# Optimization experiments

Measured on AMD Instinct MI355X. Metric: run time of the kernel, lower is better.

The kernel has to match this reference:

```python
import jax, jax.numpy as jnp
import numpy as np

B, L, D, H, UNITS = 64, 4096, 512, 512, 256

def setup_inputs() -> dict:
    key = jax.random.key(0)
    ks = jax.random.split(key, 8)
    s = lambda fan_in: 1.0 / np.sqrt(fan_in)
    return {
        "features": jax.random.normal(ks[0], (B, L, D), dtype=jnp.float32),
        "hidden": jax.random.normal(ks[1], (B, H), dtype=jnp.float32),
        "W1_k": jax.random.uniform(ks[2], (D, UNITS), jnp.float32, -s(D), s(D)),
        "W1_b": jnp.zeros((UNITS,), jnp.float32),
        "W2_k": jax.random.uniform(ks[3], (H, UNITS), jnp.float32, -s(H), s(H)),
        "W2_b": jnp.zeros((UNITS,), jnp.float32),
        "V_k": jax.random.uniform(ks[4], (UNITS, 1), jnp.float32, -s(UNITS), s(UNITS)),
        "V_b": jnp.zeros((1,), jnp.float32),
    }

def reference(features, hidden, W1_k, W1_b, W2_k, W2_b, V_k, V_b):
    # features: [B, L, D], hidden: [B, H]
    f_proj = jnp.einsum('bld,du->blu', features, W1_k) + W1_b          # [B, L, U]
    h_proj = (hidden @ W2_k + W2_b)[:, None, :]                        # [B, 1, U]
    score = jnp.einsum('blu,uo->blo', jnp.tanh(f_proj + h_proj), V_k) + V_b  # [B, L, 1]
    attention_weights = jax.nn.softmax(score, axis=1)                  # [B, L, 1]
    context_vector = jnp.sum(attention_weights * features, axis=1)     # [B, D]
    return (context_vector, attention_weights)
```

## Files before the change

kernel.cpp:

```cpp
#include <hip/hip_runtime.h>

#define Bsz 64
#define Lsz 4096
#define Dsz 512
#define Hsz 512
#define Usz 256
#define LT  64
#define NLB (Lsz / LT)

typedef __attribute__((ext_vector_type(8))) short s8v;
typedef __attribute__((ext_vector_type(4))) float f4v;
typedef __attribute__((ext_vector_type(8))) unsigned short u16x8;

#define SW(r, c) (((((c) >> 3) ^ ((r) & 7)) << 3) | ((c) & 7))

__device__ __forceinline__ unsigned short f2bf(float f) {
    unsigned int u = __float_as_uint(f);
    u += 0x7FFFu + ((u >> 16) & 1u);
    return (unsigned short)(u >> 16);
}
__device__ __forceinline__ float bf2f(unsigned int lo16) {
    return __uint_as_float(lo16 << 16);
}
__device__ __forceinline__ void barrier_lds() {
    asm volatile("s_waitcnt lgkmcnt(0)" ::: "memory");
    __builtin_amdgcn_s_barrier();
}


__global__ __launch_bounds__(256) void k_prep(const float* __restrict__ W1,
                                              const float* __restrict__ hidden,
                                              const float* __restrict__ W2,
                                              unsigned short* __restrict__ W1T,
                                              float* __restrict__ hp_part,
                                              float* __restrict__ den,
                                              float* __restrict__ ctx_acc) {
    int blk = blockIdx.x, tid = threadIdx.x;
    if (blk < 32) {
        __shared__ unsigned short Lt[64][72];
        int kb = blk >> 2, ub = blk & 3;
        {
            int rr = tid >> 2, c16 = (tid & 3) * 16;
            const float* src = W1 + (size_t)(kb * 64 + rr) * Usz + ub * 64 + c16;
            f4v v0 = *reinterpret_cast<const f4v*>(src);
            f4v v1 = *reinterpret_cast<const f4v*>(src + 4);
            f4v v2 = *reinterpret_cast<const f4v*>(src + 8);
            f4v v3 = *reinterpret_cast<const f4v*>(src + 12);
            u16x8 o0 = { f2bf(v0.x), f2bf(v0.y), f2bf(v0.z), f2bf(v0.w),
                         f2bf(v1.x), f2bf(v1.y), f2bf(v1.z), f2bf(v1.w) };
            u16x8 o1 = { f2bf(v2.x), f2bf(v2.y), f2bf(v2.z), f2bf(v2.w),
                         f2bf(v3.x), f2bf(v3.y), f2bf(v3.z), f2bf(v3.w) };
            *reinterpret_cast<u16x8*>(&Lt[rr][c16])     = o0;
            *reinterpret_cast<u16x8*>(&Lt[rr][c16 + 8]) = o1;
        }
        __syncthreads();
        {
            int ur = tid >> 2, k16 = (tid & 3) * 16;
            u16x8 o0, o1;
#pragma unroll
            for (int i = 0; i < 8; ++i) o0[i] = Lt[k16 + i][ur];
#pragma unroll
            for (int i = 0; i < 8; ++i) o1[i] = Lt[k16 + 8 + i][ur];
            unsigned short* dst = W1T + (size_t)(ub * 64 + ur) * Dsz + kb * 64 + k16;
            *reinterpret_cast<u16x8*>(dst)     = o0;
            *reinterpret_cast<u16x8*>(dst + 8) = o1;
        }
    } else if (blk < 288) {
        int idx = blk - 32;
        int kq = idx >> 6, b = idx & 63;
        const float* hrow = hidden + (size_t)b * Hsz + kq * 128;
        const float* w2p  = W2 + (size_t)(kq * 128) * Usz + tid;
        float a0 = 0.f, a1 = 0.f, a2 = 0.f, a3 = 0.f;
#pragma unroll 8
        for (int k = 0; k < 128; k += 4) {
            a0 = fmaf(hrow[k + 0], w2p[(size_t)(k + 0) * Usz], a0);
            a1 = fmaf(hrow[k + 1], w2p[(size_t)(k + 1) * Usz], a1);
            a2 = fmaf(hrow[k + 2], w2p[(size_t)(k + 2) * Usz], a2);
            a3 = fmaf(hrow[k + 3], w2p[(size_t)(k + 3) * Usz], a3);
        }
        hp_part[((size_t)kq * Bsz + b) * Usz + tid] = (a0 + a1) + (a2 + a3);
    } else {
        int b = blk - 288;
        if (tid == 0) den[b] = 0.f;
        ctx_acc[b * Dsz + tid] = 0.f;
        ctx_acc[b * Dsz + 256 + tid] = 0.f;
    }
}

__global__ void __launch_bounds__(512)
__attribute__((amdgpu_waves_per_eu(4, 4))) k_score_ctx(
    const float* __restrict__ feat, const unsigned short* __restrict__ W1T,
    const float* __restrict__ hp_part, const float* __restrict__ W1b,
    const float* __restrict__ W2b, const float* __restrict__ Vk,
    const float* __restrict__ Vb, float* __restrict__ el_arr,
    float* __restrict__ den, float* __restrict__ ctx_acc)
{
    __shared__ __align__(16) unsigned short A[LT][Dsz];
    __shared__ float hp[Usz], vv[Usz];
    __shared__ float spart[8][LT];
    __shared__ float el[LT];
    __shared__ float pc[2][Dsz];

    const int tid  = threadIdx.x;
    const int w    = tid >> 6;
    const int lane = tid & 63;
    const int lr   = lane & 15;
    const int lg   = lane >> 4;
    const int b    = blockIdx.x >> 6;
    const int lb   = blockIdx.x & 63;
    const int l0   = lb * LT;

    const int srow = tid >> 3;
    const int sfc  = (tid & 7) * 16;
    const float* fb = feat + ((size_t)b * Lsz + l0 + srow) * Dsz + sfc;

    f4v st[2][4];
#pragma unroll
    for (int i = 0; i < 4; ++i) st[0][i] = *reinterpret_cast<const f4v*>(fb + i * 4);
#pragma unroll
    for (int i = 0; i < 4; ++i) st[1][i] = *reinterpret_cast<const f4v*>(fb + 128 + i * 4);
    __builtin_amdgcn_sched_barrier(0);

    if (tid < Usz) {
        const float* hpb = hp_part + (size_t)b * Usz + tid;
        hp[tid] = (hpb[0] + hpb[Bsz * Usz]) + (hpb[2 * Bsz * Usz] + hpb[3 * Bsz * Usz])
                + W1b[tid] + W2b[tid];
        vv[tid] = Vk[tid];
    }
    {
        u16x8 o0 = { f2bf(st[0][0].x), f2bf(st[0][0].y), f2bf(st[0][0].z), f2bf(st[0][0].w),
                     f2bf(st[0][1].x), f2bf(st[0][1].y), f2bf(st[0][1].z), f2bf(st[0][1].w) };
        u16x8 o1 = { f2bf(st[0][2].x), f2bf(st[0][2].y), f2bf(st[0][2].z), f2bf(st[0][2].w),
                     f2bf(st[0][3].x), f2bf(st[0][3].y), f2bf(st[0][3].z), f2bf(st[0][3].w) };
        *reinterpret_cast<u16x8*>(&A[srow][SW(srow, sfc)])     = o0;
        *reinterpret_cast<u16x8*>(&A[srow][SW(srow, sfc + 8)]) = o1;
    }
    barrier_lds();

    const unsigned short* bp0 = W1T + (size_t)(w * 32 + lr) * Dsz + lg * 8;
    const unsigned short* bp1 = bp0 + 16 * Dsz;
    f4v acc[4][2];
#pragma unroll
    for (int mf = 0; mf < 4; ++mf) {
        acc[mf][0] = (f4v){0.f, 0.f, 0.f, 0.f};
        acc[mf][1] = (f4v){0.f, 0.f, 0.f, 0.f};
    }

#pragma unroll
    for (int c = 0; c < 4; ++c) {
        s8v bq[4][2];
#pragma unroll
        for (int k = 0; k < 4; ++k) {
            bq[k][0] = *reinterpret_cast<const s8v*>(bp0 + (c * 4 + k) * 32);
            bq[k][1] = *reinterpret_cast<const s8v*>(bp1 + (c * 4 + k) * 32);
        }
        __builtin_amdgcn_sched_barrier(0);
        if (c < 2) {
#pragma unroll
            for (int i = 0; i < 4; ++i)
                st[c & 1][i] = *reinterpret_cast<const f4v*>(fb + (c + 2) * 128 + i * 4);
        }
        __builtin_amdgcn_sched_barrier(0);
#pragma unroll
        for (int k = 0; k < 4; ++k) {
            const int kof = (c * 4 + k) * 32 + lg * 8;
#pragma unroll
            for (int mf = 0; mf < 4; ++mf) {
                const int row = mf * 16 + lr;
                s8v a = *reinterpret_cast<const s8v*>(&A[row][SW(row, kof)]);
                acc[mf][0] = __builtin_amdgcn_mfma_f32_16x16x32_bf16(a, bq[k][0], acc[mf][0], 0, 0, 0);
                acc[mf][1] = __builtin_amdgcn_mfma_f32_16x16x32_bf16(a, bq[k][1], acc[mf][1], 0, 0, 0);
            }
        }
        __builtin_amdgcn_sched_barrier(0);
        if (c < 3) {
            const int cc = (c + 1) * 128 + sfc;
            const f4v* s = st[(c + 1) & 1];
            u16x8 o0 = { f2bf(s[0].x), f2bf(s[0].y), f2bf(s[0].z), f2bf(s[0].w),
                         f2bf(s[1].x), f2bf(s[1].y), f2bf(s[1].z), f2bf(s[1].w) };
            u16x8 o1 = { f2bf(s[2].x), f2bf(s[2].y), f2bf(s[2].z), f2bf(s[2].w),
                         f2bf(s[3].x), f2bf(s[3].y), f2bf(s[3].z), f2bf(s[3].w) };
            *reinterpret_cast<u16x8*>(&A[srow][SW(srow, cc)])     = o0;
            *reinterpret_cast<u16x8*>(&A[srow][SW(srow, cc + 8)]) = o1;
            barrier_lds();
        }
    }

    {
        float rs[4][4];
#pragma unroll
        for (int mf = 0; mf < 4; ++mf)
#pragma unroll
            for (int r = 0; r < 4; ++r) rs[mf][r] = 0.f;
#pragma unroll
        for (int mf = 0; mf < 4; ++mf)
#pragma unroll
            for (int nf = 0; nf < 2; ++nf) {
                int col = w * 32 + nf * 16 + lr;
                float hpv = hp[col], vvv = vv[col];
#pragma unroll
                for (int r = 0; r < 4; ++r) {
                    float x = acc[mf][nf][r] + hpv;
                    float e = __expf(2.f * x);
                    rs[mf][r] = fmaf(1.f - 2.f / (e + 1.f), vvv, rs[mf][r]);
                }
            }
#pragma unroll
        for (int off = 1; off < 16; off <<= 1)
#pragma unroll
            for (int mf = 0; mf < 4; ++mf)
#pragma unroll
                for (int r = 0; r < 4; ++r)
                    rs[mf][r] += __shfl_xor(rs[mf][r], off, 64);
        if (lr == 0)
#pragma unroll
            for (int mf = 0; mf < 4; ++mf)
#pragma unroll
                for (int r = 0; r < 4; ++r)
                    spart[w][mf * 16 + lg * 4 + r] = rs[mf][r];
    }
    barrier_lds();

    if (tid < LT) {
        float s = Vb[0];
#pragma unroll
        for (int ww = 0; ww < 8; ++ww) s += spart[ww][tid];
        float e = __expf(s);
        el[tid] = e;
        el_arr[(size_t)b * Lsz + l0 + tid] = e;
        float es = e;
#pragma unroll
        for (int off = 1; off < 64; off <<= 1) es += __shfl_xor(es, off, 64);
        if (tid == 0) atomicAdd(&den[b], es);
    }
    barrier_lds();

    {
        const int qr = tid >> 8;
        const int d0 = (tid & 255) * 2;
        float a0 = 0.f, a1 = 0.f;
#pragma unroll 8
        for (int li = 0; li < 32; ++li) {
            int l = qr * 32 + li;
            unsigned int pk = *reinterpret_cast<const unsigned int*>(&A[l][SW(l, d0)]);
            float e = el[l];
            a0 = fmaf(e, bf2f(pk & 0xFFFFu), a0);
            a1 = fmaf(e, bf2f(pk >> 16), a1);
        }
        pc[qr][d0]     = a0;
        pc[qr][d0 + 1] = a1;
    }
    barrier_lds();
    atomicAdd(&ctx_acc[b * Dsz + tid], pc[0][tid] + pc[1][tid]);
}

__global__ __launch_bounds__(256) void k_finalize(const float* __restrict__ el_arr,
                                                  const float* __restrict__ den,
                                                  const float* __restrict__ ctx_acc,
                                                  float* __restrict__ ctx,
                                                  float* __restrict__ wout) {
    int blk = blockIdx.x, tid = threadIdx.x;
    int b = blk >> 2, q = blk & 3;
    float inv = 1.f / den[b];
    size_t base = (size_t)b * Lsz + q * 1024 + tid * 4;
    f4v e4 = *reinterpret_cast<const f4v*>(&el_arr[base]);
    f4v w4 = { e4.x * inv, e4.y * inv, e4.z * inv, e4.w * inv };
    *reinterpret_cast<f4v*>(&wout[base]) = w4;
    if (tid < 128) {
        int d = q * 128 + tid;
        ctx[(size_t)b * Dsz + d] = ctx_acc[b * Dsz + d] * inv;
    }
}

extern "C" void kernel_launch(void* const* d_in, const int* in_sizes, int n_in,
                              void* d_out, int out_size, void* d_ws, size_t ws_size,
                              hipStream_t stream) {
    const float* feat   = (const float*)d_in[0];
    const float* hidden = (const float*)d_in[1];
    const float* W1     = (const float*)d_in[2];
    const float* W1b    = (const float*)d_in[3];
    const float* W2     = (const float*)d_in[4];
    const float* W2b    = (const float*)d_in[5];
    const float* Vk     = (const float*)d_in[6];
    const float* Vb     = (const float*)d_in[7];

    unsigned short* w1t = (unsigned short*)d_ws;
    float* hp_part = (float*)((char*)d_ws + 256 * 1024);
    float* el_arr  = (float*)((char*)d_ws + 512 * 1024);
    float* den     = (float*)((char*)d_ws + 1536 * 1024);
    float* ctx_acc = (float*)((char*)d_ws + 1536 * 1024 + 256);

    float* ctx  = (float*)d_out;
    float* wout = ctx + Bsz * Dsz;

    k_prep<<<352, 256, 0, stream>>>(W1, hidden, W2, w1t, hp_part, den, ctx_acc);
    k_score_ctx<<<Bsz * NLB, 512, 0, stream>>>(feat, w1t, hp_part, W1b, W2b,
                                               Vk, Vb, el_arr, den, ctx_acc);
    k_finalize<<<Bsz * 4, 256, 0, stream>>>(el_arr, den, ctx_acc, ctx, wout);
}
```

Measured before the change: 194.6 us.

## Make score kernel persistent over 16 L-tiles with prefetched feature loads

Replaces the one-block-per-64-row grid (4096 blocks) with 512 blocks that each loop over 16 tiles of 32 rows. The next tile's features are prefetched into registers while the current tile's MFMAs run, and the W1 fragments are double-buffered. Context and denominator partials stay in registers across tiles, which cuts the number of atomics per batch. In exchange, the grid shrinks to 512 blocks, which may underfill the GPU's CUs, and each tile now pays several barriers and re-reads W1 from cache.

```diff
diff --git a/kernel.cpp b/kernel.cpp
--- a/kernel.cpp
+++ b/kernel.cpp
@@ -5,8 +5,9 @@
 #define Dsz 512
 #define Hsz 512
 #define Usz 256
-#define LT  64
-#define NLB (Lsz / LT)
+#define LT  32
+#define TPB 16
+#define NQB 8
 
 typedef __attribute__((ext_vector_type(8))) short s8v;
 typedef __attribute__((ext_vector_type(4))) float f4v;
@@ -87,6 +88,33 @@
     }
 }
 
+#define LOADB(dst, g)                                                          \
+    {                                                                          \
+        dst[0] = *reinterpret_cast<const s8v*>(bp0 + (2 * (g)) * 32);          \
+        dst[1] = *reinterpret_cast<const s8v*>(bp1 + (2 * (g)) * 32);          \
+        dst[2] = *reinterpret_cast<const s8v*>(bp0 + (2 * (g) + 1) * 32);      \
+        dst[3] = *reinterpret_cast<const s8v*>(bp1 + (2 * (g) + 1) * 32);      \
+    }
+
+#define GEMM2(ks, c0, c1)                                                      \
+    {                                                                          \
+        const int kof = (ks) * 32 + lg * 8;                                    \
+        s8v a0 = *reinterpret_cast<const s8v*>(&A[lr][SW(lr, kof)]);           \
+        s8v a1 = *reinterpret_cast<const s8v*>(&A[16 + lr][SW(16 + lr, kof)]); \
+        acc00 = __builtin_amdgcn_mfma_f32_16x16x32_bf16(a0, c0, acc00, 0, 0, 0); \
+        acc01 = __builtin_amdgcn_mfma_f32_16x16x32_bf16(a0, c1, acc01, 0, 0, 0); \
+        acc10 = __builtin_amdgcn_mfma_f32_16x16x32_bf16(a1, c0, acc10, 0, 0, 0); \
+        acc11 = __builtin_amdgcn_mfma_f32_16x16x32_bf16(a1, c1, acc11, 0, 0, 0); \
+    }
+
+#define GROUP(g, cur, nxt)                                                     \
+    {                                                                          \
+        if ((g) < 7) LOADB(nxt, (g) + 1);                                      \
+        __builtin_amdgcn_sched_barrier(0);                                     \
+        GEMM2(2 * (g),     cur[0], cur[1]);                                    \
+        GEMM2(2 * (g) + 1, cur[2], cur[3]);                                    \
+    }
+
 __global__ void __launch_bounds__(512)
 __attribute__((amdgpu_waves_per_eu(4, 4))) k_score_ctx(
     const float* __restrict__ feat, const unsigned short* __restrict__ W1T,
@@ -106,20 +134,8 @@
     const int lane = tid & 63;
     const int lr   = lane & 15;
     const int lg   = lane >> 4;
-    const int b    = blockIdx.x >> 6;
-    const int lb   = blockIdx.x & 63;
-    const int l0   = lb * LT;
-
-    const int srow = tid >> 3;
-    const int sfc  = (tid & 7) * 16;
-    const float* fb = feat + ((size_t)b * Lsz + l0 + srow) * Dsz + sfc;
-
-    f4v st[2][4];
-#pragma unroll
-    for (int i = 0; i < 4; ++i) st[0][i] = *reinterpret_cast<const f4v*>(fb + i * 4);
-#pragma unroll
-    for (int i = 0; i < 4; ++i) st[1][i] = *reinterpret_cast<const f4v*>(fb + 128 + i * 4);
-    __builtin_amdgcn_sched_barrier(0);
+    const int b    = blockIdx.x >> 3;
+    const int q8   = blockIdx.x & 7;
 
     if (tid < Usz) {
         const float* hpb = hp_part + (size_t)b * Usz + tid;
@@ -127,129 +143,134 @@
                 + W1b[tid] + W2b[tid];
         vv[tid] = Vk[tid];
     }
+
+    const int srow = tid >> 4;
+    const int sfc  = (tid & 15) * 32;
+    const float* fb = feat + ((size_t)b * Lsz + q8 * (TPB * LT) + srow) * Dsz + sfc;
+
+    f4v st[8];
+#pragma unroll
+    for (int i = 0; i < 8; ++i) st[i] = *reinterpret_cast<const f4v*>(fb + i * 4);
     {
-        u16x8 o0 = { f2bf(st[0][0].x), f2bf(st[0][0].y), f2bf(st[0][0].z), f2bf(st[0][0].w),
-                     f2bf(st[0][1].x), f2bf(st[0][1].y), f2bf(st[0][1].z), f2bf(st[0][1].w) };
-        u16x8 o1 = { f2bf(st[0][2].x), f2bf(st[0][2].y), f2bf(st[0][2].z), f2bf(st[0][2].w),
-                     f2bf(st[0][3].x), f2bf(st[0][3].y), f2bf(st[0][3].z), f2bf(st[0][3].w) };
-        *reinterpret_cast<u16x8*>(&A[srow][SW(srow, sfc)])     = o0;
-        *reinterpret_cast<u16x8*>(&A[srow][SW(srow, sfc + 8)]) = o1;
+#pragma unroll
+        for (int j = 0; j < 4; ++j) {
+            u16x8 o = { f2bf(st[2 * j].x),     f2bf(st[2 * j].y),
+                        f2bf(st[2 * j].z),     f2bf(st[2 * j].w),
+                        f2bf(st[2 * j + 1].x), f2bf(st[2 * j + 1].y),
+                        f2bf(st[2 * j + 1].z), f2bf(st[2 * j + 1].w) };
+            *reinterpret_cast<u16x8*>(&A[srow][SW(srow, sfc + j * 8)]) = o;
+        }
     }
     barrier_lds();
 
     const unsigned short* bp0 = W1T + (size_t)(w * 32 + lr) * Dsz + lg * 8;
     const unsigned short* bp1 = bp0 + 16 * Dsz;
-    f4v acc[4][2];
-#pragma unroll
-    for (int mf = 0; mf < 4; ++mf) {
-        acc[mf][0] = (f4v){0.f, 0.f, 0.f, 0.f};
-        acc[mf][1] = (f4v){0.f, 0.f, 0.f, 0.f};
-    }
-
-#pragma unroll
-    for (int c = 0; c < 4; ++c) {
-        s8v bq[4][2];
-#pragma unroll
-        for (int k = 0; k < 4; ++k) {
-            bq[k][0] = *reinterpret_cast<const s8v*>(bp0 + (c * 4 + k) * 32);
-            bq[k][1] = *reinterpret_cast<const s8v*>(bp1 + (c * 4 + k) * 32);
-        }
+
+    float cacc0 = 0.f, cacc1 = 0.f;
+    float dsum  = 0.f;
+    const int half = tid >> 8;
+    const int d0   = (tid & 255) * 2;
+
+#pragma unroll 1
+    for (int t = 0; t < TPB; ++t) {
+        f4v acc00 = (f4v){0.f, 0.f, 0.f, 0.f}, acc01 = (f4v){0.f, 0.f, 0.f, 0.f};
+        f4v acc10 = (f4v){0.f, 0.f, 0.f, 0.f}, acc11 = (f4v){0.f, 0.f, 0.f, 0.f};
+
+        s8v bq0[4], bq1[4];
+        LOADB(bq0, 0);
         __builtin_amdgcn_sched_barrier(0);
-        if (c < 2) {
-#pragma unroll
-            for (int i = 0; i < 4; ++i)
-                st[c & 1][i] = *reinterpret_cast<const f4v*>(fb + (c + 2) * 128 + i * 4);
+        if (t < TPB - 1) {
+#pragma unroll
+            for (int i = 0; i < 8; ++i)
+                st[i] = *reinterpret_cast<const f4v*>(fb + (size_t)(t + 1) * LT * Dsz + i * 4);
         }
         __builtin_amdgcn_sched_barrier(0);
-#pragma unroll
-        for (int k = 0; k < 4; ++k) {
-            const int kof = (c * 4 + k) * 32 + lg * 8;
-#pragma unroll
-            for (int mf = 0; mf < 4; ++mf) {
-                const int row = mf * 16 + lr;
-                s8v a = *reinterpret_cast<const s8v*>(&A[row][SW(row, kof)]);
-                acc[mf][0] = __builtin_amdgcn_mfma_f32_16x16x32_bf16(a, bq[k][0], acc[mf][0], 0, 0, 0);
-                acc[mf][1] = __builtin_amdgcn_mfma_f32_16x16x32_bf16(a, bq[k][1], acc[mf][1], 0, 0, 0);
-            }
-        }
-        __builtin_amdgcn_sched_barrier(0);
-        if (c < 3) {
-            const int cc = (c + 1) * 128 + sfc;
-            const f4v* s = st[(c + 1) & 1];
-            u16x8 o0 = { f2bf(s[0].x), f2bf(s[0].y), f2bf(s[0].z), f2bf(s[0].w),
-                         f2bf(s[1].x), f2bf(s[1].y), f2bf(s[1].z), f2bf(s[1].w) };
-            u16x8 o1 = { f2bf(s[2].x), f2bf(s[2].y), f2bf(s[2].z), f2bf(s[2].w),
-                         f2bf(s[3].x), f2bf(s[3].y), f2bf(s[3].z), f2bf(s[3].w) };
-            *reinterpret_cast<u16x8*>(&A[srow][SW(srow, cc)])     = o0;
-            *reinterpret_cast<u16x8*>(&A[srow][SW(srow, cc + 8)]) = o1;
-            barrier_lds();
-        }
-    }
-
-    {
-        float rs[4][4];
-#pragma unroll
-        for (int mf = 0; mf < 4; ++mf)
-#pragma unroll
-            for (int r = 0; r < 4; ++r) rs[mf][r] = 0.f;
-#pragma unroll
-        for (int mf = 0; mf < 4; ++mf)
-#pragma unroll
-            for (int nf = 0; nf < 2; ++nf) {
-                int col = w * 32 + nf * 16 + lr;
-                float hpv = hp[col], vvv = vv[col];
-#pragma unroll
-                for (int r = 0; r < 4; ++r) {
-                    float x = acc[mf][nf][r] + hpv;
+
+        GROUP(0, bq0, bq1); GROUP(1, bq1, bq0);
+        GROUP(2, bq0, bq1); GROUP(3, bq1, bq0);
+        GROUP(4, bq0, bq1); GROUP(5, bq1, bq0);
+        GROUP(6, bq0, bq1); GROUP(7, bq1, bq0);
+
+        {
+            float rs[2][4];
+#pragma unroll
+            for (int r = 0; r < 4; ++r) {
+                {
+                    int col = w * 32 + lr;
+                    float x = acc00[r] + hp[col];
                     float e = __expf(2.f * x);
-                    rs[mf][r] = fmaf(1.f - 2.f / (e + 1.f), vvv, rs[mf][r]);
+                    rs[0][r] = (1.f - 2.f / (e + 1.f)) * vv[col];
+                    x = acc01[r] + hp[col + 16];
+                    e = __expf(2.f * x);
+                    rs[0][r] = fmaf(1.f - 2.f / (e + 1.f), vv[col + 16], rs[0][r]);
+                }
+                {
+                    int col = w * 32 + lr;
+                    float x = acc10[r] + hp[col];
+                    float e = __expf(2.f * x);
+                    rs[1][r] = (1.f - 2.f / (e + 1.f)) * vv[col];
+                    x = acc11[r] + hp[col + 16];
+                    e = __expf(2.f * x);
+                    rs[1][r] = fmaf(1.f - 2.f / (e + 1.f), vv[col + 16], rs[1][r]);
                 }
             }
 #pragma unroll
-        for (int off = 1; off < 16; off <<= 1)
-#pragma unroll
-            for (int mf = 0; mf < 4; ++mf)
-#pragma unroll
-                for (int r = 0; r < 4; ++r)
-                    rs[mf][r] += __shfl_xor(rs[mf][r], off, 64);
-        if (lr == 0)
-#pragma unroll
-            for (int mf = 0; mf < 4; ++mf)
-#pragma unroll
-                for (int r = 0; r < 4; ++r)
-                    spart[w][mf * 16 + lg * 4 + r] = rs[mf][r];
-    }
-    barrier_lds();
-
-    if (tid < LT) {
-        float s = Vb[0];
-#pragma unroll
-        for (int ww = 0; ww < 8; ++ww) s += spart[ww][tid];
-        float e = __expf(s);
-        el[tid] = e;
-        el_arr[(size_t)b * Lsz + l0 + tid] = e;
-        float es = e;
-#pragma unroll
-        for (int off = 1; off < 64; off <<= 1) es += __shfl_xor(es, off, 64);
-        if (tid == 0) atomicAdd(&den[b], es);
-    }
-    barrier_lds();
-
-    {
-        const int qr = tid >> 8;
-        const int d0 = (tid & 255) * 2;
-        float a0 = 0.f, a1 = 0.f;
-#pragma unroll 8
-        for (int li = 0; li < 32; ++li) {
-            int l = qr * 32 + li;
+            for (int off = 1; off < 16; off <<= 1)
+#pragma unroll
+                for (int mf = 0; mf < 2; ++mf)
+#pragma unroll
+                    for (int r = 0; r < 4; ++r)
+                        rs[mf][r] += __shfl_xor(rs[mf][r], off, 64);
+            if (lr == 0)
+#pragma unroll
+                for (int mf = 0; mf < 2; ++mf)
+#pragma unroll
+                    for (int r = 0; r < 4; ++r)
+                        spart[w][mf * 16 + lg * 4 + r] = rs[mf][r];
+        }
+        barrier_lds();
+
+        if (tid < LT) {
+            float s = Vb[0];
+#pragma unroll
+            for (int ww = 0; ww < 8; ++ww) s += spart[ww][tid];
+            float e = __expf(s);
+            el[tid] = e;
+            el_arr[(size_t)b * Lsz + (q8 * TPB + t) * LT + tid] = e;
+            dsum += e;
+        }
+        barrier_lds();
+
+#pragma unroll
+        for (int li = 0; li < 16; ++li) {
+            int l = half * 16 + li;
             unsigned int pk = *reinterpret_cast<const unsigned int*>(&A[l][SW(l, d0)]);
             float e = el[l];
-            a0 = fmaf(e, bf2f(pk & 0xFFFFu), a0);
-            a1 = fmaf(e, bf2f(pk >> 16), a1);
-        }
-        pc[qr][d0]     = a0;
-        pc[qr][d0 + 1] = a1;
-    }
+            cacc0 = fmaf(e, bf2f(pk & 0xFFFFu), cacc0);
+            cacc1 = fmaf(e, bf2f(pk >> 16), cacc1);
+        }
+        barrier_lds();
+
+        if (t < TPB - 1) {
+#pragma unroll
+            for (int j = 0; j < 4; ++j) {
+                u16x8 o = { f2bf(st[2 * j].x),     f2bf(st[2 * j].y),
+                            f2bf(st[2 * j].z),     f2bf(st[2 * j].w),
+                            f2bf(st[2 * j + 1].x), f2bf(st[2 * j + 1].y),
+                            f2bf(st[2 * j + 1].z), f2bf(st[2 * j + 1].w) };
+                *reinterpret_cast<u16x8*>(&A[srow][SW(srow, sfc + j * 8)]) = o;
+            }
+            barrier_lds();
+        }
+    }
+
+    if (tid < LT) {
+#pragma unroll
+        for (int off = 1; off < 32; off <<= 1) dsum += __shfl_xor(dsum, off, 64);
+        if (tid == 0) atomicAdd(&den[b], dsum);
+    }
+    pc[half][d0]     = cacc0;
+    pc[half][d0 + 1] = cacc1;
     barrier_lds();
     atomicAdd(&ctx_acc[b * Dsz + tid], pc[0][tid] + pc[1][tid]);
 }
@@ -294,7 +315,7 @@
     float* wout = ctx + Bsz * Dsz;
 
     k_prep<<<352, 256, 0, stream>>>(W1, hidden, W2, w1t, hp_part, den, ctx_acc);
-    k_score_ctx<<<Bsz * NLB, 512, 0, stream>>>(feat, w1t, hp_part, W1b, W2b,
+    k_score_ctx<<<Bsz * NQB, 512, 0, stream>>>(feat, w1t, hp_part, W1b, W2b,
                                                Vk, Vb, el_arr, den, ctx_acc);
     k_finalize<<<Bsz * 4, 256, 0, stream>>>(el_arr, den, ctx_acc, ctx, wout);
 }
```

After: 409.7 us. 111% more time.
